# Performance work log

Measured on AMD Instinct MI355X. Metric: run time of the kernel, lower is better.

Reference implementation:

```python
import jax, jax.numpy as jnp
import numpy as np

B, T = 64, 500
N_EX, N_SK = 10000, 100
H, K = 128, 32


def setup_inputs() -> dict:
    key = jax.random.key(0)
    ks = jax.random.split(key, 32)
    g = lambda i, shape, s=0.05: (jax.random.normal(ks[i], shape, dtype=jnp.float32) * s)
    inp = {
        's_data': jax.random.randint(ks[0], (B, T), 0, N_SK),
        'a_data': jax.random.randint(ks[1], (B, T), 0, 2),
        'e_data': jax.random.randint(ks[2], (B, T), 0, N_EX),
        'at_data': jax.random.randint(ks[3], (B, T), 0, 100),
        'q_matrix': (jax.random.uniform(ks[4], (N_EX + 1, N_SK + 1)) < 0.05).astype(jnp.float32),
        's_embed_w': g(5, (N_SK + 1, H)),
        'a_embed_w': g(6, (2, H)),
        'e_embed_w': g(7, (N_EX + 1, H)),
        'W1': g(8, (H, 2 * H)), 'b1': jnp.zeros((H,), jnp.float32),
        'W2': g(9, (H, 3 * H)), 'b2': jnp.zeros((H,), jnp.float32),
        'W3': g(10, (H, 2 * H)), 'b3': jnp.zeros((H,), jnp.float32),
        'key_matrix': g(11, (K, H)),
        'gru_w_ih': g(12, (3 * H, H)), 'gru_w_hh': g(13, (3 * H, H)),
        'gru_b_ih': jnp.zeros((3 * H,), jnp.float32), 'gru_b_hh': jnp.zeros((3 * H,), jnp.float32),
        'Wg': g(14, (H, 2 * H)), 'bg': jnp.zeros((H,), jnp.float32),
        'Wgg': g(15, (H, 2 * H)), 'bgg': jnp.zeros((H,), jnp.float32),
        'Wf': g(16, (H, 2 * H)), 'bf': jnp.zeros((H,), jnp.float32),
        'Wp': g(17, (1, 3 * H)), 'bp': jnp.zeros((1,), jnp.float32),
        'Wp1': g(18, (1, 3 * H)), 'bp1': jnp.zeros((1,), jnp.float32),
        'h0': g(19, (H,)),           # xavier init of GRU initial state (shared across batch)
        'm0': g(20, (K, H)),         # xavier init of memory h_pre (shared across batch)
    }
    return inp


def reference(s_data, a_data, e_data, at_data, q_matrix, s_embed_w, a_embed_w, e_embed_w,
              W1, b1, W2, b2, W3, b3, key_matrix, gru_w_ih, gru_w_hh, gru_b_ih, gru_b_hh,
              Wg, bg, Wgg, bgg, Wf, bf, Wp, bp, Wp1, bp1, h0, m0):
    # eval mode: dropout = identity
    Bv, Tv = a_data.shape
    lin = lambda x, W, b: x @ W.T + b
    # ---- embedding (n_exercise > 0 branch) ----
    rel = q_matrix[e_data]                              # [B,T,S+1]
    ssum = rel.sum(-1, keepdims=True)
    ssum = jnp.where(ssum == 0, 1.0, ssum)
    s_emb = jnp.einsum('bts,sh->bth', rel, s_embed_w) / ssum
    e_emb = e_embed_w[e_data]
    a_emb = a_embed_w[a_data]
    se_data = jax.nn.relu(lin(jnp.concatenate([s_emb, e_emb], -1), W1, b1))
    se_learning = jax.nn.relu(lin(jnp.concatenate([s_emb, e_emb, a_emb], -1), W2, b2))
    e_learning = jax.nn.relu(lin(jnp.concatenate([e_emb, a_emb], -1), W3, b3))
    # ---- GRU over e_learning ----
    gx = jnp.einsum('bth,gh->btg', e_learning, gru_w_ih) + gru_b_ih  # [B,T,3H]
    def gru_step(h, gxt):
        gh = h @ gru_w_hh.T + gru_b_hh
        xr, xz, xn = jnp.split(gxt, 3, -1)
        hr, hz, hn = jnp.split(gh, 3, -1)
        r = jax.nn.sigmoid(xr + hr)
        z = jax.nn.sigmoid(xz + hz)
        n = jnp.tanh(xn + r * hn)
        hn2 = (1 - z) * n + z * h
        return hn2, hn2
    _, gru_out = jax.lax.scan(gru_step, jnp.broadcast_to(h0, (Bv, h0.shape[0])), jnp.swapaxes(gx, 0, 1))
    out = jnp.swapaxes(gru_out, 0, 1)[:, :-1]           # [B,T-1,H]
    # ---- key-value memory scan ----
    Wall = jnp.einsum('bth,kh->btk', se_data, key_matrix)  # attention weights (unnormalized)
    h_pre0 = jnp.broadcast_to(m0, (Bv,) + m0.shape)        # [B,K,H]
    ht0 = jnp.einsum('bk,bkh->bh', Wall[:, 0], h_pre0)
    xs = (jnp.swapaxes(Wall[:, :-1], 0, 1),
          jnp.swapaxes(Wall[:, 1:], 0, 1),
          jnp.swapaxes(se_learning[:, :-1], 0, 1))
    def step(carry, x):
        h_pre, ht_pre = carry
        w, w_next, learning = x
        hl = jnp.concatenate([ht_pre, learning], -1)
        gain = jnp.tanh(hl @ Wg.T + bg)
        gate = jax.nn.sigmoid(hl @ Wgg.T + bgg)
        LG = gate * gain                                  # [B,H]
        LG_t = w[:, :, None] * LG[:, None, :]             # [B,K,H] write
        gam = jax.nn.sigmoid(jnp.concatenate([h_pre, jnp.broadcast_to(LG[:, None, :], h_pre.shape)], -1) @ Wf.T + bf)
        h = gam * h_pre + LG_t
        ht = jnp.einsum('bk,bkh->bh', w_next, h)          # read at t+1
        return (h, ht), ht
    _, hts = jax.lax.scan(step, (h_pre0, ht0), xs)
    out1 = jnp.swapaxes(hts, 0, 1)                        # [B,T-1,H]
    sg = jax.lax.stop_gradient
    res = jax.nn.sigmoid(jnp.concatenate([out, sg(out1), e_emb[:, 1:]], -1) @ Wp.T + bp)[..., 0]
    res1 = jax.nn.sigmoid(jnp.concatenate([sg(out), out1, se_data[:, 1:]], -1) @ Wp1.T + bp1)[..., 0]
    pred = jnp.zeros((Bv, Tv), res.dtype).at[:, 1:].set(res * res1)
    return pred
```

## Files before the change

### kernel.cpp

```cpp
#include <hip/hip_runtime.h>

#define TT 500
typedef __attribute__((ext_vector_type(8))) short short8v;
typedef __attribute__((ext_vector_type(4))) short short4v;
typedef __attribute__((ext_vector_type(4))) float float4v;
typedef unsigned short ushort;

__device__ __forceinline__ ushort f2bf(float f) {
  union { float f; unsigned u; } v; v.f = f;
  unsigned r = v.u + 0x7FFFu + ((v.u >> 16) & 1u);
  return (ushort)(r >> 16);
}
__device__ __forceinline__ ushort f2bfr(float f) {
  union { float f; unsigned u; } v; v.f = f;
  return (ushort)((v.u + 0x8000u) >> 16);
}
__device__ __forceinline__ float bf2f(ushort u) {
  union { unsigned u; float f; } v; v.u = ((unsigned)u) << 16;
  return v.f;
}
__device__ __forceinline__ float sigm(float x) {
  return __builtin_amdgcn_rcpf(1.f + __builtin_amdgcn_exp2f(-1.44269504088896341f * x));
}
__device__ __forceinline__ float tanh_f(float x) {
  return 1.f - 2.f * __builtin_amdgcn_rcpf(1.f + __builtin_amdgcn_exp2f(2.88539008177792682f * x));
}
__device__ __forceinline__ void bar_lds() {
  asm volatile("s_waitcnt lgkmcnt(0)\ns_barrier" ::: "memory");
}
template <int CTRL>
__device__ __forceinline__ float dppadd(float v) {
  int a = __builtin_amdgcn_update_dpp(0, __builtin_bit_cast(int, v), CTRL, 0xF, 0xF, true);
  return v + __builtin_bit_cast(float, a);
}
__device__ __forceinline__ float rsum16(float v) {
  v = dppadd<0xB1>(v);
  v = dppadd<0x4E>(v);
  v = dppadd<0x141>(v);
  v = dppadd<0x140>(v);
  return v;
}
__device__ __forceinline__ void wait_flag(int* f) {
  while (__hip_atomic_load(f, __ATOMIC_RELAXED, __HIP_MEMORY_SCOPE_AGENT) == 0)
    __builtin_amdgcn_s_sleep(8);
  __builtin_amdgcn_fence(__ATOMIC_ACQUIRE, "agent");
}
#define MFMA __builtin_amdgcn_mfma_f32_16x16x32_bf16

__global__ __launch_bounds__(256) void conv_k(
    const float* __restrict__ W1, const float* __restrict__ W2,
    const float* __restrict__ W3, const float* __restrict__ Wih,
    const float* __restrict__ key, const float* __restrict__ Wg,
    const float* __restrict__ Wgg, ushort* __restrict__ wts)
{
  int idx = blockIdx.x * 256 + threadIdx.x;
  if (idx >= 200704) return;
  float v;
  if (idx < 32768)       v = W1[idx];
  else if (idx < 81920)  v = W2[idx - 32768];
  else if (idx < 114688) v = W3[idx - 81920];
  else if (idx < 163840) v = Wih[idx - 114688];
  else if (idx < 167936) v = key[idx - 163840];
  else {
    int j = idx - 167936, o = j >> 7, k = j & 127;
    v = (o < 128) ? Wg[o * 256 + 128 + k] : Wgg[(o - 128) * 256 + 128 + k];
  }
  wts[idx] = f2bf(v);
}

#define XS 424
#define SS 648

__global__ __launch_bounds__(512, 2) void mega_k(
    const int* __restrict__ a_data, const int* __restrict__ e_data,
    const float* __restrict__ qm, const float* __restrict__ semb,
    const float* __restrict__ aemb, const float* __restrict__ eemb,
    const float* __restrict__ b1, const float* __restrict__ b2,
    const float* __restrict__ b3, const float* __restrict__ bih,
    const float* __restrict__ bg, const float* __restrict__ bgg,
    const float* __restrict__ Wp, const float* __restrict__ bp,
    const float* __restrict__ Wp1, const float* __restrict__ bp1,
    const ushort* __restrict__ wts,
    const float* __restrict__ Wf, const float* __restrict__ bf_,
    const float* __restrict__ Wg, const float* __restrict__ Wgg,
    const float* __restrict__ Whh, const float* __restrict__ bhh,
    const float* __restrict__ h0v, const float* __restrict__ m0,
    ushort* __restrict__ gxb, ushort* __restrict__ xgx,
    float* __restrict__ wallb, float* __restrict__ c1b, float* __restrict__ c2b,
    ushort* __restrict__ htsm, ushort* __restrict__ htsg,
    int* __restrict__ flags)
{
  __shared__ __align__(16) ushort pool[27136];
  const int tid = threadIdx.x;
  const int w = tid >> 6, l = tid & 63, jj = l & 15, seg = l >> 4;
  const int n0 = w * 16 + seg * 4;

  if (blockIdx.x < 64) {
    __builtin_amdgcn_s_setprio(3);
    const int b = blockIdx.x;
    ushort* h_bf = pool;
    ushort* htb  = pool + 4096;
    ushort* LGb  = pool + 4224;

    short8v afrA[4], aggA[4], aggB[4], alg[4];
#pragma unroll
    for (int ks = 0; ks < 4; ++ks) {
      const float* sA = Wf  + (w * 16 + jj) * 256 + ks * 32 + seg * 8;
      const float* sB = Wg  + (w * 16 + jj) * 256 + ks * 32 + seg * 8;
      const float* sC = Wgg + (w * 16 + jj) * 256 + ks * 32 + seg * 8;
      const float* sD = Wf  + (w * 16 + jj) * 256 + 128 + ks * 32 + seg * 8;
      short8v a, bb, c, d;
#pragma unroll
      for (int j = 0; j < 8; ++j) {
        a[j] = (short)f2bf(sA[j]); bb[j] = (short)f2bf(sB[j]);
        c[j] = (short)f2bf(sC[j]); d[j] = (short)f2bf(sD[j]);
      }
      afrA[ks] = a; aggA[ks] = bb; aggB[ks] = c; alg[ks] = d;
    }
    const float4v bf4 = *(const float4v*)(bf_ + n0);

    float hreg[2][4];
#pragma unroll
    for (int nt = 0; nt < 2; ++nt) {
      int k = nt * 16 + jj;
      float4v m = *(const float4v*)(m0 + k * 128 + n0);
#pragma unroll
      for (int r = 0; r < 4; ++r) hreg[nt][r] = m[r];
      int p = ((n0 >> 3) + k) & 15;
      short4v pk;
#pragma unroll
      for (int r = 0; r < 4; ++r) pk[r] = (short)f2bf(hreg[nt][r]);
      *(short4v*)(h_bf + k * 128 + p * 8 + (n0 & 7)) = pk;
    }
    wait_flag(flags + b);
    const float* wl = wallb + (size_t)b * TT * 32;
    const ushort* xgp = xgx + (size_t)b * TT * 256;
    float wv0 = wl[jj], wv1 = wl[16 + jj];
    float wn0 = wl[32 + jj], wn1 = wl[48 + jj];
    short4v xcg  = *(const short4v*)(xgp + n0);
    short4v xcgg = *(const short4v*)(xgp + 128 + n0);
    short4v xng  = *(const short4v*)(xgp + 256 + n0);
    short4v xngg = *(const short4v*)(xgp + 384 + n0);
    {
      float4v htp;
#pragma unroll
      for (int r = 0; r < 4; ++r)
        htp[r] = rsum16(wv0 * hreg[0][r] + wv1 * hreg[1][r]);
      if (jj == 0) {
        short4v hp;
#pragma unroll
        for (int r = 0; r < 4; ++r) hp[r] = (short)f2bf(htp[r]);
        *(short4v*)(htb + n0) = hp;
      }
    }
    __syncthreads();

    for (int t = 0; t < TT - 1; ++t) {
      int tw = (t + 2 <= TT - 1) ? (t + 2) : (TT - 1);
      if ((tw & 31) == 0) wait_flag(flags + (tw >> 5) * 64 + b);
      float wf0 = wl[tw * 32 + jj], wf1 = wl[tw * 32 + 16 + jj];
      short4v xfg  = *(const short4v*)(xgp + (size_t)tw * 256 + n0);
      short4v xfgg = *(const short4v*)(xgp + (size_t)tw * 256 + 128 + n0);

      short8v hb[4];
#pragma unroll
      for (int ks = 0; ks < 4; ++ks)
        hb[ks] = *(short8v*)(htb + ks * 32 + seg * 8);

      float4v xg4, xgg4;
#pragma unroll
      for (int r = 0; r < 4; ++r) { xg4[r] = bf2f((ushort)xcg[r]); xgg4[r] = bf2f((ushort)xcgg[r]); }
      float4v dg0 = xg4, dg1 = {0,0,0,0}, gg0 = xgg4, gg1 = {0,0,0,0};
      dg0 = MFMA(aggA[0], hb[0], dg0, 0, 0, 0);
      dg0 = MFMA(aggA[1], hb[1], dg0, 0, 0, 0);
      dg1 = MFMA(aggA[2], hb[2], dg1, 0, 0, 0);
      dg1 = MFMA(aggA[3], hb[3], dg1, 0, 0, 0);
      gg0 = MFMA(aggB[0], hb[0], gg0, 0, 0, 0);
      gg0 = MFMA(aggB[1], hb[1], gg0, 0, 0, 0);
      gg1 = MFMA(aggB[2], hb[2], gg1, 0, 0, 0);
      gg1 = MFMA(aggB[3], hb[3], gg1, 0, 0, 0);

      float lgv[4];
#pragma unroll
      for (int r = 0; r < 4; ++r)
        lgv[r] = tanh_f(dg0[r] + dg1[r]) * sigm(gg0[r] + gg1[r]);
      if (jj == 0) {
        short4v lp;
#pragma unroll
        for (int r = 0; r < 4; ++r) lp[r] = (short)f2bfr(lgv[r]);
        *(short4v*)(LGb + n0) = lp;
      }

      short8v bv0[4], bv1[4];
#pragma unroll
      for (int ks = 0; ks < 4; ++ks) {
        int g = ks * 4 + seg;
        bv0[ks] = *(short8v*)(h_bf + jj * 128 + ((g + jj) & 15) * 8);
        bv1[ks] = *(short8v*)(h_bf + (16 + jj) * 128 + ((g + 16 + jj) & 15) * 8);
      }
      float4v a0A = {0,0,0,0}, a0B = {0,0,0,0}, a1A = {0,0,0,0}, a1B = {0,0,0,0};
      a0A = MFMA(afrA[0], bv0[0], a0A, 0, 0, 0);
      a0A = MFMA(afrA[1], bv0[1], a0A, 0, 0, 0);
      a0B = MFMA(afrA[2], bv0[2], a0B, 0, 0, 0);
      a0B = MFMA(afrA[3], bv0[3], a0B, 0, 0, 0);
      a1A = MFMA(afrA[0], bv1[0], a1A, 0, 0, 0);
      a1A = MFMA(afrA[1], bv1[1], a1A, 0, 0, 0);
      a1B = MFMA(afrA[2], bv1[2], a1B, 0, 0, 0);
      a1B = MFMA(afrA[3], bv1[3], a1B, 0, 0, 0);
      bar_lds();

      short8v lb[4];
#pragma unroll
      for (int ks = 0; ks < 4; ++ks)
        lb[ks] = *(short8v*)(LGb + ks * 32 + seg * 8);
      float4v dl0 = bf4, dl1 = {0,0,0,0};
      dl0 = MFMA(alg[0], lb[0], dl0, 0, 0, 0);
      dl0 = MFMA(alg[1], lb[1], dl0, 0, 0, 0);
      dl1 = MFMA(alg[2], lb[2], dl1, 0, 0, 0);
      dl1 = MFMA(alg[3], lb[3], dl1, 0, 0, 0);

      float4v htp = {0,0,0,0};
#pragma unroll
      for (int nt = 0; nt < 2; ++nt) {
        float wvv = nt ? wv1 : wv0;
        float wnn = nt ? wn1 : wn0;
#pragma unroll
        for (int r = 0; r < 4; ++r) {
          float a = nt ? (a1A[r] + a1B[r]) : (a0A[r] + a0B[r]);
          float gam = sigm(a + dl0[r] + dl1[r]);
          float hn = fmaf(gam, hreg[nt][r], wvv * lgv[r]);
          hreg[nt][r] = hn;
          htp[r] = fmaf(wnn, hn, htp[r]);
        }
        int k = nt * 16 + jj;
        int p = ((n0 >> 3) + k) & 15;
        short4v pk;
#pragma unroll
        for (int r = 0; r < 4; ++r) pk[r] = (short)f2bfr(hreg[nt][r]);
        *(short4v*)(h_bf + k * 128 + p * 8 + (n0 & 7)) = pk;
      }
#pragma unroll
      for (int r = 0; r < 4; ++r) htp[r] = rsum16(htp[r]);
      if (jj == 0) {
        short4v hp;
#pragma unroll
        for (int r = 0; r < 4; ++r) hp[r] = (short)f2bfr(htp[r]);
        *(short4v*)(htb + n0) = hp;
        *(short4v*)(htsm + ((size_t)b * TT + t) * 128 + n0) = hp;
      }
      wv0 = wn0; wv1 = wn1; wn0 = wf0; wn1 = wf1;
      xcg = xng; xcgg = xngg; xng = xfg; xngg = xfgg;
      bar_lds();
    }
  } else if (blockIdx.x < 128) {
    __builtin_amdgcn_s_setprio(3);
    const int b = blockIdx.x - 64;
    ushort* hb2 = pool;

    short8v wfr[3][4];
    float4v bfr[3];
#pragma unroll
    for (int i = 0; i < 3; ++i) {
      int Mt = w + i * 8;
#pragma unroll
      for (int ks = 0; ks < 4; ++ks) {
        const float* src = Whh + (Mt * 16 + jj) * 128 + ks * 32 + seg * 8;
        short8v tv;
#pragma unroll
        for (int j = 0; j < 8; ++j) tv[j] = (short)f2bf(src[j]);
        wfr[i][ks] = tv;
      }
      bfr[i] = *(const float4v*)(bhh + Mt * 16 + seg * 4);
    }
    float4v hj4 = *(const float4v*)(h0v + n0);
    if (jj == 0) {
      short4v hp;
#pragma unroll
      for (int r = 0; r < 4; ++r) hp[r] = (short)f2bf(hj4[r]);
      *(short4v*)(hb2 + n0) = hp;
    }
    wait_flag(flags + b);
    const ushort* gpb = gxb + (size_t)b * TT * 384;
    short4v xr_c = *(const short4v*)(gpb + n0);
    short4v xz_c = *(const short4v*)(gpb + 128 + n0);
    short4v xn_c = *(const short4v*)(gpb + 256 + n0);
    short4v xr_n = *(const short4v*)(gpb + 384 + n0);
    short4v xz_n = *(const short4v*)(gpb + 512 + n0);
    short4v xn_n = *(const short4v*)(gpb + 640 + n0);
    __syncthreads();

    for (int t = 0; t < TT - 1; ++t) {
      int tf = (t + 2 < TT - 1) ? (t + 2) : (TT - 2);
      if ((tf & 31) == 0) wait_flag(flags + (tf >> 5) * 64 + b);
      const ushort* gf = gpb + (size_t)tf * 384;
      short4v xr_f = *(const short4v*)(gf + n0);
      short4v xz_f = *(const short4v*)(gf + 128 + n0);
      short4v xn_f = *(const short4v*)(gf + 256 + n0);

      const ushort* hsrc = hb2 + (t & 1) * 128;
      short8v bfrg[4];
#pragma unroll
      for (int ks = 0; ks < 4; ++ks)
        bfrg[ks] = *(short8v*)(hsrc + ks * 32 + seg * 8);

      float4v a0A = bfr[0], a1A = bfr[1], a2A = bfr[2];
      float4v a0B = {0,0,0,0}, a1B = {0,0,0,0}, a2B = {0,0,0,0};
      a0A = MFMA(wfr[0][0], bfrg[0], a0A, 0, 0, 0);
      a0A = MFMA(wfr[0][1], bfrg[1], a0A, 0, 0, 0);
      a0B = MFMA(wfr[0][2], bfrg[2], a0B, 0, 0, 0);
      a0B = MFMA(wfr[0][3], bfrg[3], a0B, 0, 0, 0);
      a1A = MFMA(wfr[1][0], bfrg[0], a1A, 0, 0, 0);
      a1A = MFMA(wfr[1][1], bfrg[1], a1A, 0, 0, 0);
      a1B = MFMA(wfr[1][2], bfrg[2], a1B, 0, 0, 0);
      a1B = MFMA(wfr[1][3], bfrg[3], a1B, 0, 0, 0);
      a2A = MFMA(wfr[2][0], bfrg[0], a2A, 0, 0, 0);
      a2A = MFMA(wfr[2][1], bfrg[1], a2A, 0, 0, 0);
      a2B = MFMA(wfr[2][2], bfrg[2], a2B, 0, 0, 0);
      a2B = MFMA(wfr[2][3], bfrg[3], a2B, 0, 0, 0);

      ushort* hdst = hb2 + ((t + 1) & 1) * 128;
      short4v hp;
#pragma unroll
      for (int r = 0; r < 4; ++r) {
        float rr = sigm(bf2f((ushort)xr_c[r]) + a0A[r] + a0B[r]);
        float zz = sigm(bf2f((ushort)xz_c[r]) + a1A[r] + a1B[r]);
        float nn = tanh_f(bf2f((ushort)xn_c[r]) + rr * (a2A[r] + a2B[r]));
        hj4[r] = fmaf(1.f - zz, nn, zz * hj4[r]);
        hp[r] = (short)f2bfr(hj4[r]);
      }
      if (jj == 0) {
        *(short4v*)(hdst + n0) = hp;
        *(short4v*)(htsg + ((size_t)b * TT + t) * 128 + n0) = hp;
      }
      xr_c = xr_n; xz_c = xz_n; xn_c = xn_n;
      xr_n = xr_f; xz_n = xz_f; xn_n = xn_f;
      bar_lds();
    }
  } else {
    __builtin_amdgcn_s_setprio(0);
    const int gi = blockIdx.x - 128;
    const int chunk = gi >> 6, b = gi & 63;
    const int t0 = chunk * 32;
    const int NT = (TT - t0 < 32) ? (TT - t0) : 32;
    ushort* Xl = pool;
    ushort* Yl = pool + 13568;
    ushort* St = pool;
    const ushort* w1b  = wts;
    const ushort* w2b  = wts + 32768;
    const ushort* w3b  = wts + 81920;
    const ushort* wihb = wts + 114688;
    const ushort* keyb = wts + 163840;
    const ushort* wgb  = wts + 167936;

    {
      const int tok = tid >> 4, l16 = tid & 15;
      const int tsrc = (tok < NT) ? tok : (NT - 1);
      const int gt = b * TT + t0 + tsrc;
      const int e = e_data[gt], a = a_data[gt];
      const float* qrow = qm + (size_t)e * 101;
      float qv[7];
#pragma unroll
      for (int i = 0; i < 7; ++i) {
        int s = l16 + 16 * i;
        qv[i] = (s < 101) ? qrow[s] : 0.f;
      }
      const float* sbase = semb + l16 * 8;
      float4v acc0 = {0,0,0,0}, acc1 = {0,0,0,0};
      float cnt = 0.f;
#pragma unroll
      for (int i = 0; i < 7; ++i) {
        unsigned long long bal = __ballot(qv[i] != 0.f);
        unsigned m = (unsigned)((bal >> (tid & 48)) & 0xFFFFull);
        cnt += (float)__popc(m);
        while (m) {
          int s = 16 * i + __builtin_ctz(m);
          m &= m - 1;
          acc0 += *(const float4v*)(sbase + s * 128);
          acc1 += *(const float4v*)(sbase + s * 128 + 4);
        }
      }
      float inv = 1.f / fmaxf(cnt, 1.f);
      ushort* xr = Xl + tok * XS + l16 * 8;
#pragma unroll
      for (int r = 0; r < 4; ++r) { xr[r] = f2bf(acc0[r] * inv); xr[4 + r] = f2bf(acc1[r] * inv); }
      const float* ee = eemb + (size_t)e * 128 + l16 * 8;
      const float* ae = aemb + a * 128 + l16 * 8;
#pragma unroll
      for (int r = 0; r < 8; ++r) { xr[128 + r] = f2bf(ee[r]); xr[256 + r] = f2bf(ae[r]); }
    }
    __syncthreads();

    if (tid < 32) {
      int tau = tid;
      if (tau < NT) {
        const ushort* xr = Xl + tau * XS + 128;
        const float* wv = Wp + 256;
        float a0 = bp[0], a1 = 0.f, a2 = 0.f, a3 = 0.f;
        for (int j = 0; j < 128; j += 4) {
          a0 = fmaf(wv[j],     bf2f(xr[j]),     a0);
          a1 = fmaf(wv[j + 1], bf2f(xr[j + 1]), a1);
          a2 = fmaf(wv[j + 2], bf2f(xr[j + 2]), a2);
          a3 = fmaf(wv[j + 3], bf2f(xr[j + 3]), a3);
        }
        c1b[b * TT + t0 + tau] = (a0 + a1) + (a2 + a3);
      }
    }

    short8v axA[12], axB[12];
#pragma unroll
    for (int i = 0; i < 12; ++i) {
      axA[i] = *(short8v*)(Xl + jj * XS + i * 32 + seg * 8);
      axB[i] = *(short8v*)(Xl + (16 + jj) * XS + i * 32 + seg * 8);
    }

    for (int T = w; T < 24; T += 8) {
      float4v dA = {0,0,0,0}, dB = {0,0,0,0};
      float bv;
      if (T < 8) {
        const ushort* Bp = w1b + (T * 16 + jj) * 256 + seg * 8;
        bv = b1[T * 16 + jj];
#pragma unroll
        for (int k = 0; k < 8; ++k) {
          short8v bw = *(const short8v*)(Bp + k * 32);
          dA = MFMA(axA[k], bw, dA, 0, 0, 0);
          dB = MFMA(axB[k], bw, dB, 0, 0, 0);
        }
      } else if (T < 16) {
        const ushort* Bp = w2b + ((T - 8) * 16 + jj) * 384 + seg * 8;
        bv = b2[(T - 8) * 16 + jj];
#pragma unroll
        for (int k = 0; k < 12; ++k) {
          short8v bw = *(const short8v*)(Bp + k * 32);
          dA = MFMA(axA[k], bw, dA, 0, 0, 0);
          dB = MFMA(axB[k], bw, dB, 0, 0, 0);
        }
      } else {
        const ushort* Bp = w3b + ((T - 16) * 16 + jj) * 256 + seg * 8;
        bv = b3[(T - 16) * 16 + jj];
#pragma unroll
        for (int k = 0; k < 8; ++k) {
          short8v bw = *(const short8v*)(Bp + k * 32);
          dA = MFMA(axA[4 + k], bw, dA, 0, 0, 0);
          dB = MFMA(axB[4 + k], bw, dB, 0, 0, 0);
        }
      }
#pragma unroll
      for (int r = 0; r < 4; ++r) {
        float yA = dA[r] + bv, yB = dB[r] + bv;
        Yl[(seg * 4 + r) * XS + T * 16 + jj]      = f2bf(yA > 0.f ? yA : 0.f);
        Yl[(16 + seg * 4 + r) * XS + T * 16 + jj] = f2bf(yB > 0.f ? yB : 0.f);
      }
    }
    __syncthreads();

    short8v ayA[12], ayB[12];
#pragma unroll
    for (int i = 0; i < 12; ++i) {
      ayA[i] = *(short8v*)(Yl + jj * XS + i * 32 + seg * 8);
      ayB[i] = *(short8v*)(Yl + (16 + jj) * XS + i * 32 + seg * 8);
    }
    if (tid >= 32 && tid < 64) {
      int tau = tid - 32;
      if (tau < NT) {
        const ushort* xr = Yl + tau * XS;
        const float* wv = Wp1 + 256;
        float a0 = bp1[0], a1 = 0.f, a2 = 0.f, a3 = 0.f;
        for (int j = 0; j < 128; j += 4) {
          a0 = fmaf(wv[j],     bf2f(xr[j]),     a0);
          a1 = fmaf(wv[j + 1], bf2f(xr[j + 1]), a1);
          a2 = fmaf(wv[j + 2], bf2f(xr[j + 2]), a2);
          a3 = fmaf(wv[j + 3], bf2f(xr[j + 3]), a3);
        }
        c2b[b * TT + t0 + tau] = (a0 + a1) + (a2 + a3);
      }
    }
    __syncthreads();

    for (int T = w; T < 42; T += 8) {
      const ushort* Bp; int ai;
      if (T < 24)      { Bp = wihb + (T * 16 + jj) * 128 + seg * 8;        ai = 8; }
      else if (T < 40) { Bp = wgb  + ((T - 24) * 16 + jj) * 128 + seg * 8; ai = 4; }
      else             { Bp = keyb + ((T - 40) * 16 + jj) * 128 + seg * 8; ai = 0; }
      float4v dA = {0,0,0,0}, dB = {0,0,0,0};
#pragma unroll
      for (int k = 0; k < 4; ++k) {
        short8v bw = *(const short8v*)(Bp + k * 32);
        dA = MFMA(ayA[ai + k], bw, dA, 0, 0, 0);
        dB = MFMA(ayB[ai + k], bw, dB, 0, 0, 0);
      }
      if (T < 40) {
        float bv = (T < 24) ? bih[T * 16 + jj]
                 : (T < 32) ? bg[(T - 24) * 16 + jj] : bgg[(T - 32) * 16 + jj];
        int col = (T < 24) ? (T * 16 + jj) : (384 + (T - 24) * 16 + jj);
#pragma unroll
        for (int r = 0; r < 4; ++r) {
          St[(seg * 4 + r) * SS + col]      = f2bf(dA[r] + bv);
          St[(16 + seg * 4 + r) * SS + col] = f2bf(dB[r] + bv);
        }
      } else {
#pragma unroll
        for (int r = 0; r < 4; ++r) {
          int tokA = seg * 4 + r, tokB = 16 + seg * 4 + r;
          if (tokA < NT)
            wallb[((size_t)(b * TT + t0 + tokA)) * 32 + (T - 40) * 16 + jj] = dA[r];
          if (tokB < NT)
            wallb[((size_t)(b * TT + t0 + tokB)) * 32 + (T - 40) * 16 + jj] = dB[r];
        }
      }
    }
    __syncthreads();

    {
      const int tok = tid >> 4, sg = tid & 15;
      if (tok < NT) {
        size_t gt = (size_t)b * TT + t0 + tok;
#pragma unroll
        for (int p = 0; p < 3; ++p)
          *(short8v*)(gxb + gt * 384 + sg * 24 + p * 8) = *(short8v*)(St + tok * SS + sg * 24 + p * 8);
#pragma unroll
        for (int p = 0; p < 2; ++p)
          *(short8v*)(xgx + gt * 256 + sg * 16 + p * 8) = *(short8v*)(St + tok * SS + 384 + sg * 16 + p * 8);
      }
    }
    __syncthreads();
    if (tid == 0)
      __hip_atomic_store(flags + chunk * 64 + b, 1, __ATOMIC_RELEASE, __HIP_MEMORY_SCOPE_AGENT);
  }
}

__global__ __launch_bounds__(256) void combine_k(
    const ushort* __restrict__ htsg, const ushort* __restrict__ htsm,
    const float* __restrict__ c1b, const float* __restrict__ c2b,
    const float* __restrict__ Wp, const float* __restrict__ Wp1,
    float* __restrict__ out)
{
  const int b = blockIdx.x >> 2, q = blockIdx.x & 3;
  const int tid = threadIdx.x;
  const int wv = tid >> 6, l = tid & 63, slot = l >> 4, e = l & 15;
  float wpg[8], wpm[8], vpg[8], vpm[8];
#pragma unroll
  for (int r = 0; r < 8; ++r) {
    wpg[r] = Wp[e * 8 + r];  wpm[r] = Wp[128 + e * 8 + r];
    vpg[r] = Wp1[e * 8 + r]; vpm[r] = Wp1[128 + e * 8 + r];
  }
  if (q == 0 && tid == 0) out[(size_t)b * TT] = 0.f;
  const int tbeg = q * 125;
  const int tend = (tbeg + 125 < TT - 1) ? (tbeg + 125) : (TT - 1);
  for (int tau = tbeg + wv * 4 + slot; tau < tend; tau += 16) {
    size_t base = ((size_t)b * TT + tau) * 128;
    short8v hg = *(const short8v*)(htsg + base + e * 8);
    short8v hm = *(const short8v*)(htsm + base + e * 8);
    float qa = 0.f, qb = 0.f;
#pragma unroll
    for (int r = 0; r < 8; ++r) {
      float g = bf2f((ushort)hg[r]), m = bf2f((ushort)hm[r]);
      qa = fmaf(g, wpg[r], fmaf(m, wpm[r], qa));
      qb = fmaf(g, vpg[r], fmaf(m, vpm[r], qb));
    }
    qa = rsum16(qa);
    qb = rsum16(qb);
    if (e == 0) {
      size_t idx = (size_t)b * TT + tau + 1;
      out[idx] = sigm(qa + c1b[idx]) * sigm(qb + c2b[idx]);
    }
  }
}

extern "C" void kernel_launch(void* const* d_in, const int* in_sizes, int n_in,
                              void* d_out, int out_size, void* d_ws, size_t ws_size,
                              hipStream_t stream) {
  (void)in_sizes; (void)n_in; (void)out_size; (void)ws_size;
  const int* a_data = (const int*)d_in[1];
  const int* e_data = (const int*)d_in[2];
  const float* qm   = (const float*)d_in[4];
  const float* semb = (const float*)d_in[5];
  const float* aemb = (const float*)d_in[6];
  const float* eemb = (const float*)d_in[7];
  const float* W1 = (const float*)d_in[8];   const float* b1 = (const float*)d_in[9];
  const float* W2 = (const float*)d_in[10];  const float* b2 = (const float*)d_in[11];
  const float* W3 = (const float*)d_in[12];  const float* b3 = (const float*)d_in[13];
  const float* key = (const float*)d_in[14];
  const float* Wih = (const float*)d_in[15]; const float* Whh = (const float*)d_in[16];
  const float* bih = (const float*)d_in[17]; const float* bhh = (const float*)d_in[18];
  const float* Wg  = (const float*)d_in[19]; const float* bg  = (const float*)d_in[20];
  const float* Wgg = (const float*)d_in[21]; const float* bgg = (const float*)d_in[22];
  const float* Wf  = (const float*)d_in[23]; const float* bf_ = (const float*)d_in[24];
  const float* Wp  = (const float*)d_in[25]; const float* bp  = (const float*)d_in[26];
  const float* Wp1 = (const float*)d_in[27]; const float* bp1 = (const float*)d_in[28];
  const float* h0v = (const float*)d_in[29]; const float* m0  = (const float*)d_in[30];

  char* ws = (char*)d_ws;
  ushort* gxb  = (ushort*)(ws + 0);
  ushort* xgx  = (ushort*)(ws + 24576000);
  float* wallb = (float*)(ws + 40960000);
  ushort* htsm = (ushort*)(ws + 45056000);
  ushort* htsg = (ushort*)(ws + 53248000);
  float* c1b   = (float*)(ws + 61440000);
  float* c2b   = (float*)(ws + 61568000);
  ushort* wts  = (ushort*)(ws + 61696000);
  int* flags   = (int*)(ws + 62097408);
  float* out = (float*)d_out;

  hipMemsetAsync(flags, 0, 1024 * sizeof(int), stream);
  conv_k<<<dim3(784), dim3(256), 0, stream>>>(W1, W2, W3, Wih, key, Wg, Wgg, wts);
  mega_k<<<dim3(1152), dim3(512), 0, stream>>>(
      a_data, e_data, qm, semb, aemb, eemb, b1, b2, b3, bih, bg, bgg,
      Wp, bp, Wp1, bp1, wts, Wf, bf_, Wg, Wgg, Whh, bhh, h0v, m0,
      gxb, xgx, wallb, c1b, c2b, htsm, htsg, flags);
  combine_k<<<dim3(256), dim3(256), 0, stream>>>(
      htsg, htsm, c1b, c2b, Wp, Wp1, out);
}
```

Before: 833.4 us.

## Process two batch elements per recurrent block to interleave independent sequential chains

The memory-scan and GRU recurrence blocks now each handle two batch elements (b and b+32) instead of one, so the recurrent work uses 64 blocks instead of 128 and the grid shrinks accordingly. The two independent chains are interleaved within each timestep so their MFMA and transcendental latencies can overlap, sharing one barrier per step. This aims to hide the latency-bound serial chain and free CUs for the producer blocks. The cost is doubled per-step work on each recurrent block and higher register and LDS pressure.

```diff
diff --git a/kernel.cpp b/kernel.cpp
--- a/kernel.cpp
+++ b/kernel.cpp
@@ -95,12 +95,9 @@
   const int w = tid >> 6, l = tid & 63, jj = l & 15, seg = l >> 4;
   const int n0 = w * 16 + seg * 4;
 
-  if (blockIdx.x < 64) {
+  if (blockIdx.x < 32) {
     __builtin_amdgcn_s_setprio(3);
-    const int b = blockIdx.x;
-    ushort* h_bf = pool;
-    ushort* htb  = pool + 4096;
-    ushort* LGb  = pool + 4224;
+    const int b0 = blockIdx.x;
 
     short8v afrA[4], aggA[4], aggB[4], alg[4];
 #pragma unroll
@@ -119,143 +116,176 @@
     }
     const float4v bf4 = *(const float4v*)(bf_ + n0);
 
-    float hreg[2][4];
-#pragma unroll
-    for (int nt = 0; nt < 2; ++nt) {
-      int k = nt * 16 + jj;
-      float4v m = *(const float4v*)(m0 + k * 128 + n0);
-#pragma unroll
-      for (int r = 0; r < 4; ++r) hreg[nt][r] = m[r];
-      int p = ((n0 >> 3) + k) & 15;
-      short4v pk;
-#pragma unroll
-      for (int r = 0; r < 4; ++r) pk[r] = (short)f2bf(hreg[nt][r]);
-      *(short4v*)(h_bf + k * 128 + p * 8 + (n0 & 7)) = pk;
-    }
-    wait_flag(flags + b);
-    const float* wl = wallb + (size_t)b * TT * 32;
-    const ushort* xgp = xgx + (size_t)b * TT * 256;
-    float wv0 = wl[jj], wv1 = wl[16 + jj];
-    float wn0 = wl[32 + jj], wn1 = wl[48 + jj];
-    short4v xcg  = *(const short4v*)(xgp + n0);
-    short4v xcgg = *(const short4v*)(xgp + 128 + n0);
-    short4v xng  = *(const short4v*)(xgp + 256 + n0);
-    short4v xngg = *(const short4v*)(xgp + 384 + n0);
-    {
+    float hreg[2][2][4];
+#pragma unroll
+    for (int q = 0; q < 2; ++q) {
+      ushort* h_bf = pool + q * 4352;
+#pragma unroll
+      for (int nt = 0; nt < 2; ++nt) {
+        int k = nt * 16 + jj;
+        float4v m = *(const float4v*)(m0 + k * 128 + n0);
+#pragma unroll
+        for (int r = 0; r < 4; ++r) hreg[q][nt][r] = m[r];
+        int p = ((n0 >> 3) + k) & 15;
+        short4v pk;
+#pragma unroll
+        for (int r = 0; r < 4; ++r) pk[r] = (short)f2bf(hreg[q][nt][r]);
+        *(short4v*)(h_bf + k * 128 + p * 8 + (n0 & 7)) = pk;
+      }
+    }
+
+    const float* wl[2];
+    const ushort* xgp[2];
+    float wv0[2], wv1[2], wn0[2], wn1[2];
+    short4v xcg[2], xcgg[2], xng[2], xngg[2];
+#pragma unroll
+    for (int q = 0; q < 2; ++q) {
+      const int b = b0 + q * 32;
+      wait_flag(flags + b);
+      wl[q]  = wallb + (size_t)b * TT * 32;
+      xgp[q] = xgx + (size_t)b * TT * 256;
+      wv0[q] = wl[q][jj];      wv1[q] = wl[q][16 + jj];
+      wn0[q] = wl[q][32 + jj]; wn1[q] = wl[q][48 + jj];
+      xcg[q]  = *(const short4v*)(xgp[q] + n0);
+      xcgg[q] = *(const short4v*)(xgp[q] + 128 + n0);
+      xng[q]  = *(const short4v*)(xgp[q] + 256 + n0);
+      xngg[q] = *(const short4v*)(xgp[q] + 384 + n0);
       float4v htp;
 #pragma unroll
       for (int r = 0; r < 4; ++r)
-        htp[r] = rsum16(wv0 * hreg[0][r] + wv1 * hreg[1][r]);
+        htp[r] = rsum16(wv0[q] * hreg[q][0][r] + wv1[q] * hreg[q][1][r]);
       if (jj == 0) {
         short4v hp;
 #pragma unroll
         for (int r = 0; r < 4; ++r) hp[r] = (short)f2bf(htp[r]);
-        *(short4v*)(htb + n0) = hp;
+        *(short4v*)(pool + q * 4352 + 4096 + n0) = hp;
       }
     }
     __syncthreads();
 
     for (int t = 0; t < TT - 1; ++t) {
       int tw = (t + 2 <= TT - 1) ? (t + 2) : (TT - 1);
-      if ((tw & 31) == 0) wait_flag(flags + (tw >> 5) * 64 + b);
-      float wf0 = wl[tw * 32 + jj], wf1 = wl[tw * 32 + 16 + jj];
-      short4v xfg  = *(const short4v*)(xgp + (size_t)tw * 256 + n0);
-      short4v xfgg = *(const short4v*)(xgp + (size_t)tw * 256 + 128 + n0);
-
-      short8v hb[4];
-#pragma unroll
-      for (int ks = 0; ks < 4; ++ks)
-        hb[ks] = *(short8v*)(htb + ks * 32 + seg * 8);
-
-      float4v xg4, xgg4;
-#pragma unroll
-      for (int r = 0; r < 4; ++r) { xg4[r] = bf2f((ushort)xcg[r]); xgg4[r] = bf2f((ushort)xcgg[r]); }
-      float4v dg0 = xg4, dg1 = {0,0,0,0}, gg0 = xgg4, gg1 = {0,0,0,0};
-      dg0 = MFMA(aggA[0], hb[0], dg0, 0, 0, 0);
-      dg0 = MFMA(aggA[1], hb[1], dg0, 0, 0, 0);
-      dg1 = MFMA(aggA[2], hb[2], dg1, 0, 0, 0);
-      dg1 = MFMA(aggA[3], hb[3], dg1, 0, 0, 0);
-      gg0 = MFMA(aggB[0], hb[0], gg0, 0, 0, 0);
-      gg0 = MFMA(aggB[1], hb[1], gg0, 0, 0, 0);
-      gg1 = MFMA(aggB[2], hb[2], gg1, 0, 0, 0);
-      gg1 = MFMA(aggB[3], hb[3], gg1, 0, 0, 0);
-
-      float lgv[4];
-#pragma unroll
-      for (int r = 0; r < 4; ++r)
-        lgv[r] = tanh_f(dg0[r] + dg1[r]) * sigm(gg0[r] + gg1[r]);
-      if (jj == 0) {
-        short4v lp;
-#pragma unroll
-        for (int r = 0; r < 4; ++r) lp[r] = (short)f2bfr(lgv[r]);
-        *(short4v*)(LGb + n0) = lp;
-      }
-
-      short8v bv0[4], bv1[4];
-#pragma unroll
-      for (int ks = 0; ks < 4; ++ks) {
-        int g = ks * 4 + seg;
-        bv0[ks] = *(short8v*)(h_bf + jj * 128 + ((g + jj) & 15) * 8);
-        bv1[ks] = *(short8v*)(h_bf + (16 + jj) * 128 + ((g + 16 + jj) & 15) * 8);
-      }
-      float4v a0A = {0,0,0,0}, a0B = {0,0,0,0}, a1A = {0,0,0,0}, a1B = {0,0,0,0};
-      a0A = MFMA(afrA[0], bv0[0], a0A, 0, 0, 0);
-      a0A = MFMA(afrA[1], bv0[1], a0A, 0, 0, 0);
-      a0B = MFMA(afrA[2], bv0[2], a0B, 0, 0, 0);
-      a0B = MFMA(afrA[3], bv0[3], a0B, 0, 0, 0);
-      a1A = MFMA(afrA[0], bv1[0], a1A, 0, 0, 0);
-      a1A = MFMA(afrA[1], bv1[1], a1A, 0, 0, 0);
-      a1B = MFMA(afrA[2], bv1[2], a1B, 0, 0, 0);
-      a1B = MFMA(afrA[3], bv1[3], a1B, 0, 0, 0);
+      float wf0[2], wf1[2];
+      short4v xfg[2], xfgg[2];
+      float lgv[2][4];
+      float4v a0A[2], a0B[2], a1A[2], a1B[2];
+
+#pragma unroll
+      for (int q = 0; q < 2; ++q) {
+        const int b = b0 + q * 32;
+        ushort* h_bf = pool + q * 4352;
+        ushort* htb  = h_bf + 4096;
+        ushort* LGb  = h_bf + 4224;
+        if ((tw & 31) == 0) wait_flag(flags + (tw >> 5) * 64 + b);
+        wf0[q] = wl[q][tw * 32 + jj]; wf1[q] = wl[q][tw * 32 + 16 + jj];
+        xfg[q]  = *(const short4v*)(xgp[q] + (size_t)tw * 256 + n0);
+        xfgg[q] = *(const short4v*)(xgp[q] + (size_t)tw * 256 + 128 + n0);
+
+        short8v hb[4];
+#pragma unroll
+        for (int ks = 0; ks < 4; ++ks)
+          hb[ks] = *(short8v*)(htb + ks * 32 + seg * 8);
+
+        float4v xg4, xgg4;
+#pragma unroll
+        for (int r = 0; r < 4; ++r) {
+          xg4[r] = bf2f((ushort)xcg[q][r]);
+          xgg4[r] = bf2f((ushort)xcgg[q][r]);
+        }
+        float4v dg0 = xg4, dg1 = {0,0,0,0}, gg0 = xgg4, gg1 = {0,0,0,0};
+        dg0 = MFMA(aggA[0], hb[0], dg0, 0, 0, 0);
+        dg0 = MFMA(aggA[1], hb[1], dg0, 0, 0, 0);
+        dg1 = MFMA(aggA[2], hb[2], dg1, 0, 0, 0);
+        dg1 = MFMA(aggA[3], hb[3], dg1, 0, 0, 0);
+        gg0 = MFMA(aggB[0], hb[0], gg0, 0, 0, 0);
+        gg0 = MFMA(aggB[1], hb[1], gg0, 0, 0, 0);
+        gg1 = MFMA(aggB[2], hb[2], gg1, 0, 0, 0);
+        gg1 = MFMA(aggB[3], hb[3], gg1, 0, 0, 0);
+
+#pragma unroll
+        for (int r = 0; r < 4; ++r)
+          lgv[q][r] = tanh_f(dg0[r] + dg1[r]) * sigm(gg0[r] + gg1[r]);
+        if (jj == 0) {
+          short4v lp;
+#pragma unroll
+          for (int r = 0; r < 4; ++r) lp[r] = (short)f2bfr(lgv[q][r]);
+          *(short4v*)(LGb + n0) = lp;
+        }
+
+        short8v bv0[4], bv1[4];
+#pragma unroll
+        for (int ks = 0; ks < 4; ++ks) {
+          int g = ks * 4 + seg;
+          bv0[ks] = *(short8v*)(h_bf + jj * 128 + ((g + jj) & 15) * 8);
+          bv1[ks] = *(short8v*)(h_bf + (16 + jj) * 128 + ((g + 16 + jj) & 15) * 8);
+        }
+        float4v z = {0,0,0,0};
+        a0A[q] = z; a0B[q] = z; a1A[q] = z; a1B[q] = z;
+        a0A[q] = MFMA(afrA[0], bv0[0], a0A[q], 0, 0, 0);
+        a0A[q] = MFMA(afrA[1], bv0[1], a0A[q], 0, 0, 0);
+        a0B[q] = MFMA(afrA[2], bv0[2], a0B[q], 0, 0, 0);
+        a0B[q] = MFMA(afrA[3], bv0[3], a0B[q], 0, 0, 0);
+        a1A[q] = MFMA(afrA[0], bv1[0], a1A[q], 0, 0, 0);
+        a1A[q] = MFMA(afrA[1], bv1[1], a1A[q], 0, 0, 0);
+        a1B[q] = MFMA(afrA[2], bv1[2], a1B[q], 0, 0, 0);
+        a1B[q] = MFMA(afrA[3], bv1[3], a1B[q], 0, 0, 0);
+      }
       bar_lds();
 
-      short8v lb[4];
-#pragma unroll
-      for (int ks = 0; ks < 4; ++ks)
-        lb[ks] = *(short8v*)(LGb + ks * 32 + seg * 8);
-      float4v dl0 = bf4, dl1 = {0,0,0,0};
-      dl0 = MFMA(alg[0], lb[0], dl0, 0, 0, 0);
-      dl0 = MFMA(alg[1], lb[1], dl0, 0, 0, 0);
-      dl1 = MFMA(alg[2], lb[2], dl1, 0, 0, 0);
-      dl1 = MFMA(alg[3], lb[3], dl1, 0, 0, 0);
-
-      float4v htp = {0,0,0,0};
-#pragma unroll
-      for (int nt = 0; nt < 2; ++nt) {
-        float wvv = nt ? wv1 : wv0;
-        float wnn = nt ? wn1 : wn0;
-#pragma unroll
-        for (int r = 0; r < 4; ++r) {
-          float a = nt ? (a1A[r] + a1B[r]) : (a0A[r] + a0B[r]);
-          float gam = sigm(a + dl0[r] + dl1[r]);
-          float hn = fmaf(gam, hreg[nt][r], wvv * lgv[r]);
-          hreg[nt][r] = hn;
-          htp[r] = fmaf(wnn, hn, htp[r]);
-        }
-        int k = nt * 16 + jj;
-        int p = ((n0 >> 3) + k) & 15;
-        short4v pk;
-#pragma unroll
-        for (int r = 0; r < 4; ++r) pk[r] = (short)f2bfr(hreg[nt][r]);
-        *(short4v*)(h_bf + k * 128 + p * 8 + (n0 & 7)) = pk;
-      }
-#pragma unroll
-      for (int r = 0; r < 4; ++r) htp[r] = rsum16(htp[r]);
-      if (jj == 0) {
-        short4v hp;
-#pragma unroll
-        for (int r = 0; r < 4; ++r) hp[r] = (short)f2bfr(htp[r]);
-        *(short4v*)(htb + n0) = hp;
-        *(short4v*)(htsm + ((size_t)b * TT + t) * 128 + n0) = hp;
-      }
-      wv0 = wn0; wv1 = wn1; wn0 = wf0; wn1 = wf1;
-      xcg = xng; xcgg = xngg; xng = xfg; xngg = xfgg;
+#pragma unroll
+      for (int q = 0; q < 2; ++q) {
+        const int b = b0 + q * 32;
+        ushort* h_bf = pool + q * 4352;
+        ushort* htb  = h_bf + 4096;
+        ushort* LGb  = h_bf + 4224;
+
+        short8v lb[4];
+#pragma unroll
+        for (int ks = 0; ks < 4; ++ks)
+          lb[ks] = *(short8v*)(LGb + ks * 32 + seg * 8);
+        float4v dl0 = bf4, dl1 = {0,0,0,0};
+        dl0 = MFMA(alg[0], lb[0], dl0, 0, 0, 0);
+        dl0 = MFMA(alg[1], lb[1], dl0, 0, 0, 0);
+        dl1 = MFMA(alg[2], lb[2], dl1, 0, 0, 0);
+        dl1 = MFMA(alg[3], lb[3], dl1, 0, 0, 0);
+
+        float4v htp = {0,0,0,0};
+#pragma unroll
+        for (int nt = 0; nt < 2; ++nt) {
+          float wvv = nt ? wv1[q] : wv0[q];
+          float wnn = nt ? wn1[q] : wn0[q];
+#pragma unroll
+          for (int r = 0; r < 4; ++r) {
+            float a = nt ? (a1A[q][r] + a1B[q][r]) : (a0A[q][r] + a0B[q][r]);
+            float gam = sigm(a + dl0[r] + dl1[r]);
+            float hn = fmaf(gam, hreg[q][nt][r], wvv * lgv[q][r]);
+            hreg[q][nt][r] = hn;
+            htp[r] = fmaf(wnn, hn, htp[r]);
+          }
+          int k = nt * 16 + jj;
+          int p = ((n0 >> 3) + k) & 15;
+          short4v pk;
+#pragma unroll
+          for (int r = 0; r < 4; ++r) pk[r] = (short)f2bfr(hreg[q][nt][r]);
+          *(short4v*)(h_bf + k * 128 + p * 8 + (n0 & 7)) = pk;
+        }
+#pragma unroll
+        for (int r = 0; r < 4; ++r) htp[r] = rsum16(htp[r]);
+        if (jj == 0) {
+          short4v hp;
+#pragma unroll
+          for (int r = 0; r < 4; ++r) hp[r] = (short)f2bfr(htp[r]);
+          *(short4v*)(htb + n0) = hp;
+          *(short4v*)(htsm + ((size_t)b * TT + t) * 128 + n0) = hp;
+        }
+        wv0[q] = wn0[q]; wv1[q] = wn1[q]; wn0[q] = wf0[q]; wn1[q] = wf1[q];
+        xcg[q] = xng[q]; xcgg[q] = xngg[q]; xng[q] = xfg[q]; xngg[q] = xfgg[q];
+      }
       bar_lds();
     }
-  } else if (blockIdx.x < 128) {
+  } else if (blockIdx.x < 64) {
     __builtin_amdgcn_s_setprio(3);
-    const int b = blockIdx.x - 64;
-    ushort* hb2 = pool;
+    const int b0 = blockIdx.x - 32;
 
     short8v wfr[3][4];
     float4v bfr[3];
@@ -272,73 +302,89 @@
       }
       bfr[i] = *(const float4v*)(bhh + Mt * 16 + seg * 4);
     }
-    float4v hj4 = *(const float4v*)(h0v + n0);
-    if (jj == 0) {
-      short4v hp;
-#pragma unroll
-      for (int r = 0; r < 4; ++r) hp[r] = (short)f2bf(hj4[r]);
-      *(short4v*)(hb2 + n0) = hp;
-    }
-    wait_flag(flags + b);
-    const ushort* gpb = gxb + (size_t)b * TT * 384;
-    short4v xr_c = *(const short4v*)(gpb + n0);
-    short4v xz_c = *(const short4v*)(gpb + 128 + n0);
-    short4v xn_c = *(const short4v*)(gpb + 256 + n0);
-    short4v xr_n = *(const short4v*)(gpb + 384 + n0);
-    short4v xz_n = *(const short4v*)(gpb + 512 + n0);
-    short4v xn_n = *(const short4v*)(gpb + 640 + n0);
+
+    float4v hj4[2];
+    const ushort* gpb[2];
+    short4v xr_c[2], xz_c[2], xn_c[2], xr_n[2], xz_n[2], xn_n[2];
+#pragma unroll
+    for (int q = 0; q < 2; ++q) {
+      hj4[q] = *(const float4v*)(h0v + n0);
+      if (jj == 0) {
+        short4v hp;
+#pragma unroll
+        for (int r = 0; r < 4; ++r) hp[r] = (short)f2bf(hj4[q][r]);
+        *(short4v*)(pool + q * 256 + n0) = hp;
+      }
+    }
+#pragma unroll
+    for (int q = 0; q < 2; ++q) {
+      const int b = b0 + q * 32;
+      wait_flag(flags + b);
+      gpb[q] = gxb + (size_t)b * TT * 384;
+      xr_c[q] = *(const short4v*)(gpb[q] + n0);
+      xz_c[q] = *(const short4v*)(gpb[q] + 128 + n0);
+      xn_c[q] = *(const short4v*)(gpb[q] + 256 + n0);
+      xr_n[q] = *(const short4v*)(gpb[q] + 384 + n0);
+      xz_n[q] = *(const short4v*)(gpb[q] + 512 + n0);
+      xn_n[q] = *(const short4v*)(gpb[q] + 640 + n0);
+    }
     __syncthreads();
 
     for (int t = 0; t < TT - 1; ++t) {
       int tf = (t + 2 < TT - 1) ? (t + 2) : (TT - 2);
-      if ((tf & 31) == 0) wait_flag(flags + (tf >> 5) * 64 + b);
-      const ushort* gf = gpb + (size_t)tf * 384;
-      short4v xr_f = *(const short4v*)(gf + n0);
-      short4v xz_f = *(const short4v*)(gf + 128 + n0);
-      short4v xn_f = *(const short4v*)(gf + 256 + n0);
-
-      const ushort* hsrc = hb2 + (t & 1) * 128;
-      short8v bfrg[4];
-#pragma unroll
-      for (int ks = 0; ks < 4; ++ks)
-        bfrg[ks] = *(short8v*)(hsrc + ks * 32 + seg * 8);
-
-      float4v a0A = bfr[0], a1A = bfr[1], a2A = bfr[2];
-      float4v a0B = {0,0,0,0}, a1B = {0,0,0,0}, a2B = {0,0,0,0};
-      a0A = MFMA(wfr[0][0], bfrg[0], a0A, 0, 0, 0);
-      a0A = MFMA(wfr[0][1], bfrg[1], a0A, 0, 0, 0);
-      a0B = MFMA(wfr[0][2], bfrg[2], a0B, 0, 0, 0);
-      a0B = MFMA(wfr[0][3], bfrg[3], a0B, 0, 0, 0);
-      a1A = MFMA(wfr[1][0], bfrg[0], a1A, 0, 0, 0);
-      a1A = MFMA(wfr[1][1], bfrg[1], a1A, 0, 0, 0);
-      a1B = MFMA(wfr[1][2], bfrg[2], a1B, 0, 0, 0);
-      a1B = MFMA(wfr[1][3], bfrg[3], a1B, 0, 0, 0);
-      a2A = MFMA(wfr[2][0], bfrg[0], a2A, 0, 0, 0);
-      a2A = MFMA(wfr[2][1], bfrg[1], a2A, 0, 0, 0);
-      a2B = MFMA(wfr[2][2], bfrg[2], a2B, 0, 0, 0);
-      a2B = MFMA(wfr[2][3], bfrg[3], a2B, 0, 0, 0);
-
-      ushort* hdst = hb2 + ((t + 1) & 1) * 128;
-      short4v hp;
-#pragma unroll
-      for (int r = 0; r < 4; ++r) {
-        float rr = sigm(bf2f((ushort)xr_c[r]) + a0A[r] + a0B[r]);
-        float zz = sigm(bf2f((ushort)xz_c[r]) + a1A[r] + a1B[r]);
-        float nn = tanh_f(bf2f((ushort)xn_c[r]) + rr * (a2A[r] + a2B[r]));
-        hj4[r] = fmaf(1.f - zz, nn, zz * hj4[r]);
-        hp[r] = (short)f2bfr(hj4[r]);
-      }
-      if (jj == 0) {
-        *(short4v*)(hdst + n0) = hp;
-        *(short4v*)(htsg + ((size_t)b * TT + t) * 128 + n0) = hp;
-      }
-      xr_c = xr_n; xz_c = xz_n; xn_c = xn_n;
-      xr_n = xr_f; xz_n = xz_f; xn_n = xn_f;
+#pragma unroll
+      for (int q = 0; q < 2; ++q) {
+        const int b = b0 + q * 32;
+        if ((tf & 31) == 0) wait_flag(flags + (tf >> 5) * 64 + b);
+        const ushort* gf = gpb[q] + (size_t)tf * 384;
+        short4v xr_f = *(const short4v*)(gf + n0);
+        short4v xz_f = *(const short4v*)(gf + 128 + n0);
+        short4v xn_f = *(const short4v*)(gf + 256 + n0);
+
+        ushort* hb2 = pool + q * 256;
+        const ushort* hsrc = hb2 + (t & 1) * 128;
+        short8v bfrg[4];
+#pragma unroll
+        for (int ks = 0; ks < 4; ++ks)
+          bfrg[ks] = *(short8v*)(hsrc + ks * 32 + seg * 8);
+
+        float4v a0A = bfr[0], a1A = bfr[1], a2A = bfr[2];
+        float4v a0B = {0,0,0,0}, a1B = {0,0,0,0}, a2B = {0,0,0,0};
+        a0A = MFMA(wfr[0][0], bfrg[0], a0A, 0, 0, 0);
+        a0A = MFMA(wfr[0][1], bfrg[1], a0A, 0, 0, 0);
+        a0B = MFMA(wfr[0][2], bfrg[2], a0B, 0, 0, 0);
+        a0B = MFMA(wfr[0][3], bfrg[3], a0B, 0, 0, 0);
+        a1A = MFMA(wfr[1][0], bfrg[0], a1A, 0, 0, 0);
+        a1A = MFMA(wfr[1][1], bfrg[1], a1A, 0, 0, 0);
+        a1B = MFMA(wfr[1][2], bfrg[2], a1B, 0, 0, 0);
+        a1B = MFMA(wfr[1][3], bfrg[3], a1B, 0, 0, 0);
+        a2A = MFMA(wfr[2][0], bfrg[0], a2A, 0, 0, 0);
+        a2A = MFMA(wfr[2][1], bfrg[1], a2A, 0, 0, 0);
+        a2B = MFMA(wfr[2][2], bfrg[2], a2B, 0, 0, 0);
+        a2B = MFMA(wfr[2][3], bfrg[3], a2B, 0, 0, 0);
+
+        ushort* hdst = hb2 + ((t + 1) & 1) * 128;
+        short4v hp;
+#pragma unroll
+        for (int r = 0; r < 4; ++r) {
+          float rr = sigm(bf2f((ushort)xr_c[q][r]) + a0A[r] + a0B[r]);
+          float zz = sigm(bf2f((ushort)xz_c[q][r]) + a1A[r] + a1B[r]);
+          float nn = tanh_f(bf2f((ushort)xn_c[q][r]) + rr * (a2A[r] + a2B[r]));
+          hj4[q][r] = fmaf(1.f - zz, nn, zz * hj4[q][r]);
+          hp[r] = (short)f2bfr(hj4[q][r]);
+        }
+        if (jj == 0) {
+          *(short4v*)(hdst + n0) = hp;
+          *(short4v*)(htsg + ((size_t)b * TT + t) * 128 + n0) = hp;
+        }
+        xr_c[q] = xr_n[q]; xz_c[q] = xz_n[q]; xn_c[q] = xn_n[q];
+        xr_n[q] = xr_f; xz_n[q] = xz_f; xn_n[q] = xn_f;
+      }
       bar_lds();
     }
   } else {
     __builtin_amdgcn_s_setprio(0);
-    const int gi = blockIdx.x - 128;
+    const int gi = blockIdx.x - 64;
     const int chunk = gi >> 6, b = gi & 63;
     const int t0 = chunk * 32;
     const int NT = (TT - t0 < 32) ? (TT - t0) : 32;
@@ -603,7 +649,7 @@
 
   hipMemsetAsync(flags, 0, 1024 * sizeof(int), stream);
   conv_k<<<dim3(784), dim3(256), 0, stream>>>(W1, W2, W3, Wih, key, Wg, Wgg, wts);
-  mega_k<<<dim3(1152), dim3(512), 0, stream>>>(
+  mega_k<<<dim3(1088), dim3(512), 0, stream>>>(
       a_data, e_data, qm, semb, aemb, eemb, b1, b2, b3, bih, bg, bgg,
       Wp, bp, Wp1, bp1, wts, Wf, bf_, Wg, Wgg, Whh, bhh, h0v, m0,
       gxb, xgx, wallb, c1b, c2b, htsm, htsg, flags);
```

New measurement: 1.368 ms. 64.1% more time.
